# Kernel optimization log

Measured on AMD Instinct MI355X. Metric: run time of the kernel, lower is better.

## Reference

```python
import jax, jax.numpy as jnp
import numpy as np

SEQ = 4096
BLOCK = 64
NUM_RAND = 3
B, H, D = 1, 12, 64


def _build_bigbird_mask(seq_len=SEQ, block=BLOCK, num_rand=NUM_RAND, seed=0):
    """Dense [S,S] BigBird mask: global first/last block, window +-1 block,
    num_rand random blocks per middle row (mirrors bigbird_block_rand_mask)."""
    nb = seq_len // block
    rng = np.random.RandomState(seed)
    m = np.zeros((nb, nb), dtype=np.int32)
    # global blocks (first & last block attend/are attended everywhere)
    m[0, :] = 1
    m[-1, :] = 1
    m[:, 0] = 1
    m[:, -1] = 1
    # sliding window of one block on each side
    idx = np.arange(nb)
    win = np.abs(idx[:, None] - idx[None, :]) <= 1
    m[win] = 1
    # random blocks for middle rows, excluding window and global columns
    for i in range(1, nb - 1):
        cand = np.array([j for j in range(1, nb - 1) if abs(j - i) > 1], dtype=np.int32)
        sel = rng.permutation(cand)[:num_rand]
        m[i, sel] = 1
    return np.kron(m, np.ones((block, block), dtype=np.int32))


def setup_inputs() -> dict:
    key = jax.random.key(0)
    kq, kk, kv = jax.random.split(key, 3)
    q = jax.random.normal(kq, (B, H, SEQ, D), dtype=jnp.float32)
    k = jax.random.normal(kk, (B, H, SEQ, D), dtype=jnp.float32)
    v = jax.random.normal(kv, (B, H, SEQ, D), dtype=jnp.float32)
    mask = jnp.asarray(_build_bigbird_mask(), dtype=jnp.int32)  # [S, S]
    return {"q": q, "k": k, "v": v, "mask": mask}


def reference(q, k, v, mask):
    # OriginalFullAttention with dense BigBird mask:
    # scores = QK^T / sqrt(D); masked positions get -10000 additive bias.
    scale = 1.0 / np.sqrt(D).astype(np.float32)
    scores = jnp.einsum("bhqd,bhkd->bhqk", q, k) * scale
    adder = (1.0 - mask.astype(scores.dtype)) * jnp.asarray(-10000.0, scores.dtype)
    probs = jax.nn.softmax(scores + adder[None, None, :, :], axis=-1)
    out = jnp.einsum("bhqk,bhkd->bhqd", probs, v)  # [B, H, S, D]
    return out
```

## Files before the change

kernel.cpp:

```cpp
#include <hip/hip_runtime.h>
#include <stdint.h>

#define SEQ 4096
#define DH  64
#define NB  64
#define NH  12

typedef float  f32x4   __attribute__((ext_vector_type(4)));
typedef float  f32x16  __attribute__((ext_vector_type(16)));
typedef short  s16x8   __attribute__((ext_vector_type(8)));
typedef unsigned short ushort_t;
typedef unsigned long long u64;

__device__ __forceinline__ unsigned short f2bf(float x){
    union { float f; unsigned u; } c; c.f = x;
    unsigned u = c.u;
    u += 0x7fffu + ((u >> 16) & 1u);
    return (unsigned short)(u >> 16);
}

__device__ __forceinline__ unsigned pk2(float lo, float hi){
    return (unsigned)f2bf(lo) | ((unsigned)f2bf(hi) << 16);
}

__device__ __forceinline__ s16x8 pack8(f32x4 a, f32x4 b){
    s16x8 r;
#pragma unroll
    for (int i = 0; i < 4; ++i) { r[i] = (short)f2bf(a[i]); r[i+4] = (short)f2bf(b[i]); }
    return r;
}

__device__ __forceinline__ int swz(int row, int col){
    return row * 64 + (col ^ ((row & 7) << 3));
}

#define GLOAD_LDS(gp, lp) __builtin_amdgcn_global_load_lds( \
    (const __attribute__((address_space(1))) unsigned int*)(gp), \
    (__attribute__((address_space(3))) unsigned int*)(lp), 16, 0, 0)

#define KBF_OFF   0
#define VTB_OFF   6291456
#define PART_OFF  12582912
#define BMP_OFF   15777792
#define WS_NEED   15778304
#define SLOT_F    4160

__global__ __launch_bounds__(256) void bb_conv(
        const float* __restrict__ k, const float* __restrict__ v,
        const int* __restrict__ mask,
        ushort_t* __restrict__ kbf, ushort_t* __restrict__ vtb,
        u64* __restrict__ bmp)
{
    const int kb = blockIdx.x, h = blockIdx.y;
    const int tid = threadIdx.x;
    __shared__ float vls[64*65];

    if (h == 0 && tid < 64){
        bool a = mask[(size_t)(kb*64)*SEQ + tid*64] != 0;
        u64 bm = __ballot(a);
        if (tid == 0) bmp[kb] = bm;
    }

    const int j = tid >> 2, c = (tid & 3) * 16;
    const size_t gsrc = (size_t)h*SEQ*DH + (size_t)(kb*64 + j)*DH + c;
    const size_t tdst = ((size_t)h*NB + kb) * 4096;

    {
        f32x4 a0 = *(const f32x4*)(k + gsrc);
        f32x4 a1 = *(const f32x4*)(k + gsrc + 4);
        f32x4 a2 = *(const f32x4*)(k + gsrc + 8);
        f32x4 a3 = *(const f32x4*)(k + gsrc + 12);
        *(s16x8*)&kbf[tdst + swz(j, c    )] = pack8(a0, a1);
        *(s16x8*)&kbf[tdst + swz(j, c + 8)] = pack8(a2, a3);
    }
    {
        f32x4 b0 = *(const f32x4*)(v + gsrc);
        f32x4 b1 = *(const f32x4*)(v + gsrc + 4);
        f32x4 b2 = *(const f32x4*)(v + gsrc + 8);
        f32x4 b3 = *(const f32x4*)(v + gsrc + 12);
#pragma unroll
        for (int i = 0; i < 4; ++i){
            vls[j*65 + c + i     ] = b0[i];
            vls[j*65 + c + 4 + i ] = b1[i];
            vls[j*65 + c + 8 + i ] = b2[i];
            vls[j*65 + c + 12 + i] = b3[i];
        }
    }
    __syncthreads();
    {
        const int d = tid >> 2, jc = (tid & 3) * 16;
        s16x8 r0, r1;
#pragma unroll
        for (int i = 0; i < 8; ++i){
            r0[i] = (short)f2bf(vls[(jc + i    )*65 + d]);
            r1[i] = (short)f2bf(vls[(jc + i + 8)*65 + d]);
        }
        *(s16x8*)&vtb[tdst + swz(d, jc    )] = r0;
        *(s16x8*)&vtb[tdst + swz(d, jc + 8)] = r1;
    }
}

__global__ __launch_bounds__(256) void bb_main(
        const float* __restrict__ q,
        const ushort_t* __restrict__ kbf, const ushort_t* __restrict__ vtb,
        const u64* __restrict__ bmp,
        float* __restrict__ out, float* __restrict__ part)
{
    const int lin = blockIdx.x;
    const int job = (lin & 7) * 117 + (lin >> 3);
    const int h   = job / 78;
    const int x   = job - h * 78;

    int qb, wq = -1, sp = 0; u64 rmask;
    if (x < 62) { qb = x + 1; rmask = ~0ull; }
    else { int e = x - 62; wq = e >> 3; sp = e & 7; qb = wq ? 63 : 0; rmask = 0xFFull << (sp*8); }

    const int tid  = threadIdx.x;
    const int wave = tid >> 6;
    const int lane = tid & 63;
    const int l31  = lane & 31;
    const int hi   = lane >> 5;
    const int qh   = wave >> 1;
    const int kh   = wave & 1;

    __shared__ __align__(16) ushort_t KV[3][2][4096];
    __shared__ float lsm[64];

    const size_t hoff = (size_t)h * SEQ * DH;

    s16x8 qf[4];
    {
        const float sc = 0.125f * 1.4426950408889634f;
        const float* qp = q + hoff + (size_t)(qb*64 + qh*32 + l31) * DH + 8*hi;
#pragma unroll
        for (int c = 0; c < 4; ++c){
            f32x4 a = *(const f32x4*)(qp + c*16);
            f32x4 b = *(const f32x4*)(qp + c*16 + 4);
            a *= sc; b *= sc;
            qf[c] = pack8(a, b);
        }
    }

    u64 bits = bmp[qb] & rmask;

    const ushort_t* Kb = kbf + (size_t)h * (NB*4096);
    const ushort_t* Vb = vtb + (size_t)h * (NB*4096);

    f32x16 oa0 = {0.f}, oa1 = {0.f};
    float lp = 0.f;

    const int soff = wave*1024 + lane*16;
#define STAGE(gbase, lbase)                                          \
    {                                                                \
        const char* g0 = (const char*)(gbase) + soff;                \
        char*       l0 = (char*)(lbase) + wave*1024;                 \
        GLOAD_LDS(g0, l0);                                           \
        GLOAD_LDS(g0 + 4096, l0 + 4096);                             \
    }

    if (bits){
        const int n = __popcll(bits);
        u64 bpre = bits;

        int kb0 = __builtin_ctzll(bpre); bpre &= bpre - 1;
        STAGE(Kb + (size_t)kb0*4096, &KV[0][0][0]);
        STAGE(Vb + (size_t)kb0*4096, &KV[0][1][0]);
        int kb1 = 0;
        if (bpre){ kb1 = __builtin_ctzll(bpre); bpre &= bpre - 1; }
        STAGE(Kb + (size_t)kb1*4096, &KV[1][0][0]);
        STAGE(Vb + (size_t)kb1*4096, &KV[1][1][0]);

        int buf = 0;
        for (int t = 0; t < n; ++t){
            asm volatile("s_waitcnt vmcnt(4)" ::: "memory");
            __builtin_amdgcn_s_barrier();

            {
                int kbn = 0;
                if (bpre){ kbn = __builtin_ctzll(bpre); bpre &= bpre - 1; }
                int b2 = buf + 2; if (b2 >= 3) b2 -= 3;
                STAGE(Kb + (size_t)kbn*4096, &KV[b2][0][0]);
                STAGE(Vb + (size_t)kbn*4096, &KV[b2][1][0]);
            }

            const ushort_t* Kt = &KV[buf][0][0];
            const ushort_t* Vt = &KV[buf][1][0];

            f32x16 sa = {0.f};
            __builtin_amdgcn_s_setprio(1);
#pragma unroll
            for (int c = 0; c < 4; ++c){
                s16x8 kf = *(const s16x8*)&Kt[swz(kh*32 + l31, c*16 + 8*hi)];
                sa = __builtin_amdgcn_mfma_f32_32x32x16_bf16(kf, qf[c], sa, 0, 0, 0);
            }
            __builtin_amdgcn_s_setprio(0);

            float p[16];
#pragma unroll
            for (int r = 0; r < 16; ++r){
                p[r] = __builtin_amdgcn_exp2f(sa[r]);
                lp += p[r];
            }

            s16x8 pa[2];
#pragma unroll
            for (int s = 0; s < 2; ++s){
                unsigned a1 = pk2(p[8*s+0], p[8*s+1]);
                unsigned b1 = pk2(p[8*s+4], p[8*s+5]);
                unsigned a2 = pk2(p[8*s+2], p[8*s+3]);
                unsigned b2 = pk2(p[8*s+6], p[8*s+7]);
                asm("v_permlane32_swap_b32 %0, %1" : "+v"(a1), "+v"(b1));
                asm("v_permlane32_swap_b32 %0, %1" : "+v"(a2), "+v"(b2));
                union { unsigned w[4]; s16x8 v; } u;
                u.w[0] = a1; u.w[1] = a2; u.w[2] = b1; u.w[3] = b2;
                pa[s] = u.v;
            }

            __builtin_amdgcn_s_setprio(1);
#pragma unroll
            for (int s = 0; s < 2; ++s){
                s16x8 v0 = *(const s16x8*)&Vt[swz(     l31, kh*32 + s*16 + 8*hi)];
                s16x8 v1 = *(const s16x8*)&Vt[swz(32 + l31, kh*32 + s*16 + 8*hi)];
                oa0 = __builtin_amdgcn_mfma_f32_32x32x16_bf16(pa[s], v0, oa0, 0, 0, 0);
                oa1 = __builtin_amdgcn_mfma_f32_32x32x16_bf16(pa[s], v1, oa1, 0, 0, 0);
            }
            __builtin_amdgcn_s_setprio(0);

            ++buf; if (buf >= 3) buf -= 3;
        }
    }
#undef STAGE

    float lpf = lp + __shfl_xor(lp, 32);

    __syncthreads();
    float* msm = (float*)&KV[0][0][0];

    if (kh == 1){
#pragma unroll
        for (int r = 0; r < 16; ++r){
            const int cr = (r&3) + 8*(r>>2) + 4*hi;
            msm[(qh*32 + cr)*64 +      l31] = oa0[r];
            msm[(qh*32 + cr)*64 + 32 + l31] = oa1[r];
        }
        if (lane < 32) lsm[qh*32 + lane] = lpf;
    }
    __syncthreads();

    if (kh == 0){
        const float lt = lpf + lsm[qh*32 + l31];
        if (wq < 0){
            const float inv = lt > 0.f ? 1.0f / lt : 0.f;
            float* op = out + hoff + (size_t)(qb*64 + qh*32) * DH;
#pragma unroll
            for (int r = 0; r < 16; ++r){
                const int cr = (r&3) + 8*(r>>2) + 4*hi;
                const float ir = __shfl(inv, cr);
                op[(size_t)cr*DH +      l31] = (oa0[r] + msm[(qh*32 + cr)*64 +      l31]) * ir;
                op[(size_t)cr*DH + 32 + l31] = (oa1[r] + msm[(qh*32 + cr)*64 + 32 + l31]) * ir;
            }
        } else {
            float* pp = part + ((size_t)(h*2 + wq)*8 + sp) * SLOT_F;
#pragma unroll
            for (int r = 0; r < 16; ++r){
                const int cr = (r&3) + 8*(r>>2) + 4*hi;
                pp[(qh*32 + cr)*64 +      l31] = oa0[r] + msm[(qh*32 + cr)*64 +      l31];
                pp[(qh*32 + cr)*64 + 32 + l31] = oa1[r] + msm[(qh*32 + cr)*64 + 32 + l31];
            }
            if (lane < 32) pp[4096 + qh*32 + lane] = lt;
        }
    }
}

__global__ __launch_bounds__(256) void bb_comb(
        const float* __restrict__ part, float* __restrict__ out)
{
    const int h = blockIdx.x >> 1, wq = blockIdx.x & 1;
    const int qb = wq ? 63 : 0;
    const int tid = threadIdx.x;
    const int i = tid >> 2, cg = (tid & 3) * 16;

    const float* base = part + (size_t)(h*2 + wq) * 8 * SLOT_F;
    f32x4 acc[4] = {{0,0,0,0},{0,0,0,0},{0,0,0,0},{0,0,0,0}};
    float ls = 0.f;
#pragma unroll
    for (int s = 0; s < 8; ++s){
        const float* p = base + (size_t)s * SLOT_F;
#pragma unroll
        for (int c4 = 0; c4 < 4; ++c4)
            acc[c4] += *(const f32x4*)(p + (size_t)i*DH + cg + c4*4);
        ls += p[4096 + i];
    }
    const float inv = ls > 0.f ? 1.0f / ls : 0.f;
    float* op = out + (size_t)h*SEQ*DH + (size_t)(qb*64 + i)*DH + cg;
#pragma unroll
    for (int c4 = 0; c4 < 4; ++c4){
        f32x4 r = acc[c4] * inv;
        *(f32x4*)(op + c4*4) = r;
    }
}

__global__ __launch_bounds__(256) void bb_attn_fb(
        const float* __restrict__ q, const float* __restrict__ k,
        const float* __restrict__ v, const int* __restrict__ mask,
        float* __restrict__ out)
{
    const int qb   = blockIdx.x;
    const int h    = blockIdx.y;
    const int tid  = threadIdx.x;
    const int wave = tid >> 6;
    const int lane = tid & 63;
    const int lrow = lane & 15;
    const int lgrp = lane >> 4;

    __shared__ __align__(16) ushort_t Kb[64*64];
    __shared__ __align__(16) ushort_t Vt[64*64];
    __shared__ __align__(16) ushort_t Pw[4][16*64];

    const size_t hoff = (size_t)h * SEQ * DH;
    const int qrow = qb*64 + wave*16 + lrow;
    const float* qp = q + hoff + (size_t)qrow * DH + lgrp*8;
    s16x8 qf[2];
#pragma unroll
    for (int kc = 0; kc < 2; ++kc){
        f32x4 a = *(const f32x4*)(qp + kc*32);
        f32x4 b = *(const f32x4*)(qp + kc*32 + 4);
        a *= 0.125f; b *= 0.125f;
        qf[kc] = pack8(a, b);
    }
    const f32x4 zero = {0.f,0.f,0.f,0.f};
    f32x4 oa[4] = {zero, zero, zero, zero};
    float m_run[4] = {-1e30f,-1e30f,-1e30f,-1e30f};
    float l_run[4] = {0.f,0.f,0.f,0.f};
    const int* mrow = mask + (size_t)(qb*64) * SEQ;
    const int kr  = tid >> 2, kcg  = tid & 3;
    const int j2  = tid >> 3, dgrp = tid & 7;

    for (int kb = 0; kb < NB; ++kb){
        if (mrow[kb*64] == 0) continue;
        __syncthreads();
        {
            const float* kp = k + hoff + (size_t)(kb*64 + kr) * DH + kcg*16;
            f32x4 a0 = *(const f32x4*)(kp);
            f32x4 a1 = *(const f32x4*)(kp+4);
            f32x4 a2 = *(const f32x4*)(kp+8);
            f32x4 a3 = *(const f32x4*)(kp+12);
            *(s16x8*)&Kb[(kr*64) + (kcg*16     ^ ((kr&7)<<3))] = pack8(a0, a1);
            *(s16x8*)&Kb[(kr*64) + ((kcg*16+8) ^ ((kr&7)<<3))] = pack8(a2, a3);
        }
        {
            const float* vp0 = v + hoff + (size_t)(kb*64 + 2*j2) * DH + dgrp*8;
            f32x4 b0 = *(const f32x4*)(vp0);
            f32x4 b1 = *(const f32x4*)(vp0+4);
            f32x4 b2 = *(const f32x4*)(vp0+DH);
            f32x4 b3 = *(const f32x4*)(vp0+DH+4);
            float r0[8] = {b0[0],b0[1],b0[2],b0[3],b1[0],b1[1],b1[2],b1[3]};
            float r1[8] = {b2[0],b2[1],b2[2],b2[3],b3[0],b3[1],b3[2],b3[3]};
#pragma unroll
            for (int i = 0; i < 8; ++i){
                int dd = (i + dgrp) & 7;
                int d  = dgrp*8 + dd;
                unsigned val = (unsigned)f2bf(r0[dd]) | ((unsigned)f2bf(r1[dd]) << 16);
                *(unsigned*)&Vt[(d*64) + (2*j2 ^ ((d&7)<<3))] = val;
            }
        }
        __syncthreads();
        f32x4 sa[4] = {zero, zero, zero, zero};
#pragma unroll
        for (int jt = 0; jt < 4; ++jt)
#pragma unroll
            for (int kc = 0; kc < 2; ++kc){
                int row = jt*16 + lrow, col = kc*32 + lgrp*8;
                s16x8 kf = *(const s16x8*)&Kb[row*64 + (col ^ ((row&7)<<3))];
                sa[jt] = __builtin_amdgcn_mfma_f32_16x16x32_bf16(qf[kc], kf, sa[jt], 0, 0, 0);
            }
        float fac[4];
#pragma unroll
        for (int r = 0; r < 4; ++r){
            float mx = fmaxf(fmaxf(sa[0][r], sa[1][r]), fmaxf(sa[2][r], sa[3][r]));
            mx = fmaxf(mx, __shfl_xor(mx, 1));
            mx = fmaxf(mx, __shfl_xor(mx, 2));
            mx = fmaxf(mx, __shfl_xor(mx, 4));
            mx = fmaxf(mx, __shfl_xor(mx, 8));
            float mn = fmaxf(m_run[r], mx);
            fac[r] = __expf(m_run[r] - mn);
            m_run[r] = mn;
        }
#pragma unroll
        for (int r = 0; r < 4; ++r){
            float p0 = __expf(sa[0][r] - m_run[r]);
            float p1 = __expf(sa[1][r] - m_run[r]);
            float p2 = __expf(sa[2][r] - m_run[r]);
            float p3 = __expf(sa[3][r] - m_run[r]);
            sa[0][r]=p0; sa[1][r]=p1; sa[2][r]=p2; sa[3][r]=p3;
            float sm = p0+p1+p2+p3;
            sm += __shfl_xor(sm, 1);
            sm += __shfl_xor(sm, 2);
            sm += __shfl_xor(sm, 4);
            sm += __shfl_xor(sm, 8);
            l_run[r] = l_run[r]*fac[r] + sm;
        }
#pragma unroll
        for (int dc = 0; dc < 4; ++dc)
#pragma unroll
            for (int r = 0; r < 4; ++r) oa[dc][r] *= fac[r];
#pragma unroll
        for (int jt = 0; jt < 4; ++jt)
#pragma unroll
            for (int r = 0; r < 4; ++r){
                int row = lgrp*4 + r, col = jt*16 + lrow;
                Pw[wave][row*64 + (col ^ ((row&7)<<3))] = f2bf(sa[jt][r]);
            }
        s16x8 pf0 = *(const s16x8*)&Pw[wave][lrow*64 + ((     lgrp*8) ^ ((lrow&7)<<3))];
        s16x8 pf1 = *(const s16x8*)&Pw[wave][lrow*64 + ((32 + lgrp*8) ^ ((lrow&7)<<3))];
#pragma unroll
        for (int dc = 0; dc < 4; ++dc){
            int row0 = dc*16 + lrow;
            s16x8 v0 = *(const s16x8*)&Vt[row0*64 + ((     lgrp*8) ^ ((row0&7)<<3))];
            s16x8 v1 = *(const s16x8*)&Vt[row0*64 + ((32 + lgrp*8) ^ ((row0&7)<<3))];
            oa[dc] = __builtin_amdgcn_mfma_f32_16x16x32_bf16(pf0, v0, oa[dc], 0, 0, 0);
            oa[dc] = __builtin_amdgcn_mfma_f32_16x16x32_bf16(pf1, v1, oa[dc], 0, 0, 0);
        }
    }
    float inv[4];
#pragma unroll
    for (int r = 0; r < 4; ++r) inv[r] = 1.0f / l_run[r];
    float* op = out + hoff + (size_t)(qb*64 + wave*16) * DH;
#pragma unroll
    for (int dc = 0; dc < 4; ++dc)
#pragma unroll
        for (int r = 0; r < 4; ++r)
            op[(size_t)(lgrp*4 + r) * DH + dc*16 + lrow] = oa[dc][r] * inv[r];
}

extern "C" void kernel_launch(void* const* d_in, const int* in_sizes, int n_in,
                              void* d_out, int out_size, void* d_ws, size_t ws_size,
                              hipStream_t stream)
{
    const float* q    = (const float*)d_in[0];
    const float* k    = (const float*)d_in[1];
    const float* v    = (const float*)d_in[2];
    const int*   mask = (const int*)d_in[3];
    float* out = (float*)d_out;

    if (ws_size < (size_t)WS_NEED){
        dim3 grid(NB, NH, 1);
        bb_attn_fb<<<grid, 256, 0, stream>>>(q, k, v, mask, out);
        return;
    }

    char* ws = (char*)d_ws;
    ushort_t* kbf = (ushort_t*)(ws + KBF_OFF);
    ushort_t* vtb = (ushort_t*)(ws + VTB_OFF);
    float*    prt = (float*)   (ws + PART_OFF);
    u64*      bmp = (u64*)     (ws + BMP_OFF);

    bb_conv<<<dim3(NB, NH, 1), 256, 0, stream>>>(k, v, mask, kbf, vtb, bmp);
    bb_main<<<dim3(936, 1, 1), 256, 0, stream>>>(q, kbf, vtb, bmp, out, prt);
    bb_comb<<<dim3(24, 1, 1), 256, 0, stream>>>(prt, out);
}
```

Measured before the change: 40.58 us.

## Switch to double-buffered K/V staging and hardware bf16 pack conversion

Replaces the three-stage K/V LDS ring with a two-buffer scheme: only one block is prefetched ahead, the wait becomes vmcnt(0), and the prefetch is skipped when no blocks remain. This cuts LDS use from 48KB to 32KB per workgroup, which can allow more workgroups per CU, and drops the useless dummy loads. It also swaps the software round-to-nearest bf16 packing of probabilities for the v_cvt_pk_bf16_f32 instruction. The risk is a shallower prefetch pipeline, since each iteration now waits for all outstanding loads.

```diff
diff --git a/kernel.cpp b/kernel.cpp
--- a/kernel.cpp
+++ b/kernel.cpp
@@ -19,8 +19,10 @@
     return (unsigned short)(u >> 16);
 }
 
-__device__ __forceinline__ unsigned pk2(float lo, float hi){
-    return (unsigned)f2bf(lo) | ((unsigned)f2bf(hi) << 16);
+__device__ __forceinline__ unsigned cvtpk(float lo, float hi){
+    unsigned r;
+    asm("v_cvt_pk_bf16_f32 %0, %1, %2" : "=v"(r) : "v"(lo), "v"(hi));
+    return r;
 }
 
 __device__ __forceinline__ s16x8 pack8(f32x4 a, f32x4 b){
@@ -123,7 +125,7 @@
     const int qh   = wave >> 1;
     const int kh   = wave & 1;
 
-    __shared__ __align__(16) ushort_t KV[3][2][4096];
+    __shared__ __align__(16) ushort_t KV[2][2][4096];
     __shared__ float lsm[64];
 
     const size_t hoff = (size_t)h * SEQ * DH;
@@ -165,22 +167,16 @@
         int kb0 = __builtin_ctzll(bpre); bpre &= bpre - 1;
         STAGE(Kb + (size_t)kb0*4096, &KV[0][0][0]);
         STAGE(Vb + (size_t)kb0*4096, &KV[0][1][0]);
-        int kb1 = 0;
-        if (bpre){ kb1 = __builtin_ctzll(bpre); bpre &= bpre - 1; }
-        STAGE(Kb + (size_t)kb1*4096, &KV[1][0][0]);
-        STAGE(Vb + (size_t)kb1*4096, &KV[1][1][0]);
 
         int buf = 0;
         for (int t = 0; t < n; ++t){
-            asm volatile("s_waitcnt vmcnt(4)" ::: "memory");
+            asm volatile("s_waitcnt vmcnt(0)" ::: "memory");
             __builtin_amdgcn_s_barrier();
 
-            {
-                int kbn = 0;
-                if (bpre){ kbn = __builtin_ctzll(bpre); bpre &= bpre - 1; }
-                int b2 = buf + 2; if (b2 >= 3) b2 -= 3;
-                STAGE(Kb + (size_t)kbn*4096, &KV[b2][0][0]);
-                STAGE(Vb + (size_t)kbn*4096, &KV[b2][1][0]);
+            if (bpre){
+                int kbn = __builtin_ctzll(bpre); bpre &= bpre - 1;
+                STAGE(Kb + (size_t)kbn*4096, &KV[buf^1][0][0]);
+                STAGE(Vb + (size_t)kbn*4096, &KV[buf^1][1][0]);
             }
 
             const ushort_t* Kt = &KV[buf][0][0];
@@ -205,10 +201,10 @@
             s16x8 pa[2];
 #pragma unroll
             for (int s = 0; s < 2; ++s){
-                unsigned a1 = pk2(p[8*s+0], p[8*s+1]);
-                unsigned b1 = pk2(p[8*s+4], p[8*s+5]);
-                unsigned a2 = pk2(p[8*s+2], p[8*s+3]);
-                unsigned b2 = pk2(p[8*s+6], p[8*s+7]);
+                unsigned a1 = cvtpk(p[8*s+0], p[8*s+1]);
+                unsigned b1 = cvtpk(p[8*s+4], p[8*s+5]);
+                unsigned a2 = cvtpk(p[8*s+2], p[8*s+3]);
+                unsigned b2 = cvtpk(p[8*s+6], p[8*s+7]);
                 asm("v_permlane32_swap_b32 %0, %1" : "+v"(a1), "+v"(b1));
                 asm("v_permlane32_swap_b32 %0, %1" : "+v"(a2), "+v"(b2));
                 union { unsigned w[4]; s16x8 v; } u;
@@ -226,7 +222,7 @@
             }
             __builtin_amdgcn_s_setprio(0);
 
-            ++buf; if (buf >= 3) buf -= 3;
+            buf ^= 1;
         }
     }
 #undef STAGE
```

Measured after the change: 37.64 us. -7.2%, faster.
